# Performance work log

Measured on AMD Instinct MI355X. Metric: run time of the kernel, lower is better.

## Reference

```python
import jax, jax.numpy as jnp
import numpy as np

GROUPS = 32
HEADS = 8
EPS = 1e-5


def setup_inputs() -> dict:
    key = jax.random.key(0)
    ks = jax.random.split(key, 3)
    b, c, h, w = 8, 512, 32, 32
    x = jax.random.normal(ks[0], (b, c, h, w), dtype=jnp.float32)
    gn_w = jnp.ones((c,), jnp.float32)
    gn_b = jnp.zeros((c,), jnp.float32)
    qkv_w = jax.random.normal(ks[1], (3 * c, c), dtype=jnp.float32) * (1.0 / np.sqrt(c))
    qkv_b = jnp.zeros((3 * c,), jnp.float32)
    proj_w = jax.random.normal(ks[2], (c, c), dtype=jnp.float32) * (1.0 / np.sqrt(c))
    proj_b = jnp.zeros((c,), jnp.float32)
    return {"x": x, "gn_w": gn_w, "gn_b": gn_b, "qkv_w": qkv_w,
            "qkv_b": qkv_b, "proj_w": proj_w, "proj_b": proj_b}


def group_norm(x, weight, bias):
    b, c, h, w = x.shape
    xg = x.reshape(b, GROUPS, c // GROUPS, h, w)
    mean = xg.mean(axis=(2, 3, 4), keepdims=True)
    var = xg.var(axis=(2, 3, 4), keepdims=True)
    xn = ((xg - mean) * jax.lax.rsqrt(var + EPS)).reshape(b, c, h, w)
    return xn * weight[None, :, None, None] + bias[None, :, None, None]


def reference(x, gn_w, gn_b, qkv_w, qkv_b, proj_w, proj_b):
    b, c, h, w = x.shape
    dh = c // HEADS
    xn = group_norm(x, gn_w, gn_b)
    # 1x1 conv == per-pixel linear: (b,c,h,w) x (3c,c) -> (b,3c,h,w)
    qkv = jnp.einsum('bchw,oc->bohw', xn, qkv_w) + qkv_b[None, :, None, None]
    qkv = qkv.reshape(b, 3, HEADS, dh, h * w)  # 'three' outermost, then heads, head_dim
    q, k, v = qkv[:, 0], qkv[:, 1], qkv[:, 2]  # (b, heads, dh, hw)
    scale = dh ** (-0.5)
    attn = jax.nn.softmax(jnp.einsum('bhci,bhcj->bhij', q, k) * scale, axis=-1)
    out = jnp.einsum('bhij,bhcj->bhci', attn, v)  # (b, heads, dh, hw)
    out = out.reshape(b, c, h, w)
    out = jnp.einsum('bchw,oc->bohw', out, proj_w) + proj_b[None, :, None, None]
    return x + out
```

## Files before the change

### kernel.cpp

```cpp
#include <hip/hip_runtime.h>
#include <cstdint>
#include <cstddef>

#define BATCH 8
#define CCH   512
#define SSP   1024
#define NH    8
#define DH    64
#define O3    1536

typedef __bf16 bf16x8 __attribute__((ext_vector_type(8)));
typedef float  f32x4  __attribute__((ext_vector_type(4)));

__device__ __forceinline__ unsigned short f2bf(float f) {
    unsigned u = __builtin_bit_cast(unsigned, f);
    unsigned r = u + 0x7fffu + ((u >> 16) & 1u);
    return (unsigned short)(r >> 16);
}

__device__ __forceinline__ unsigned pk2bf(float lo, float hi) {
    unsigned ul = __builtin_bit_cast(unsigned, lo) + 0x8000u;
    unsigned uh = __builtin_bit_cast(unsigned, hi) + 0x8000u;
    return __builtin_amdgcn_perm(uh, ul, 0x07060302u);
}

__device__ __forceinline__ bf16x8 ld8(const unsigned short* p) {
    uint4 u = *(const uint4*)p;
    return __builtin_bit_cast(bf16x8, u);
}

__device__ __forceinline__ void glls16(const void* g, void* l) {
    __builtin_amdgcn_global_load_lds(
        (const __attribute__((address_space(1))) unsigned*)g,
        (__attribute__((address_space(3))) unsigned*)l, 16, 0, 0);
}

__global__ __launch_bounds__(256) void gn_wconv(const float* __restrict__ x,
                                                const float* __restrict__ gw,
                                                const float* __restrict__ gb,
                                                unsigned short* __restrict__ xnt,
                                                const float* __restrict__ s1,
                                                unsigned short* __restrict__ d1, int n1,
                                                const float* __restrict__ s2,
                                                unsigned short* __restrict__ d2) {
    int t = threadIdx.x;
    if (blockIdx.x >= 256) {
        int i = (blockIdx.x - 256) * 256 + t;
        const float4* sp;
        ushort4* dp;
        if (i < n1) { sp = (const float4*)s1 + i; dp = (ushort4*)d1 + i; }
        else        { sp = (const float4*)s2 + (i - n1); dp = (ushort4*)d2 + (i - n1); }
        float4 v = *sp;
        ushort4 o;
        o.x = f2bf(v.x); o.y = f2bf(v.y); o.z = f2bf(v.z); o.w = f2bf(v.w);
        *dp = o;
        return;
    }

    int blk = blockIdx.x;
    int b = blk >> 5, g = blk & 31;
    const float4* xp = (const float4*)(x + (size_t)(b * CCH + g * 16) * SSP);

    float4 vals[16];
    float sum = 0.f, ss = 0.f;
#pragma unroll
    for (int i = 0; i < 16; i++) {
        float4 v = xp[i * 256 + t];
        vals[i] = v;
        sum += (v.x + v.y) + (v.z + v.w);
        ss  += (v.x * v.x + v.y * v.y) + (v.z * v.z + v.w * v.w);
    }
#pragma unroll
    for (int o = 32; o; o >>= 1) {
        sum += __shfl_xor(sum, o, 64);
        ss  += __shfl_xor(ss,  o, 64);
    }
    __shared__ float red[8];
    if ((t & 63) == 0) { red[(t >> 6) * 2] = sum; red[(t >> 6) * 2 + 1] = ss; }
    __syncthreads();
    sum = red[0] + red[2] + red[4] + red[6];
    ss  = red[1] + red[3] + red[5] + red[7];

    float mean = sum * (1.f / 16384.f);
    float var  = ss * (1.f / 16384.f) - mean * mean;
    float rstd = rsqrtf(var + 1e-5f);

    __shared__ unsigned short tile[16][1032];
#pragma unroll
    for (int i = 0; i < 16; i++) {
        int f4 = i * 256 + t;
        int c = f4 >> 8;
        int s = (f4 & 255) * 4;
        float wsc = gw[g * 16 + c] * rstd;
        float bia = gb[g * 16 + c] - mean * wsc;
        float4 v = vals[i];
        tile[c][s + 0] = f2bf(v.x * wsc + bia);
        tile[c][s + 1] = f2bf(v.y * wsc + bia);
        tile[c][s + 2] = f2bf(v.z * wsc + bia);
        tile[c][s + 3] = f2bf(v.w * wsc + bia);
    }
    __syncthreads();

    int c2 = (t & 7) * 2, sr = t >> 3;
    unsigned short* outbase = xnt + (size_t)b * SSP * CCH + g * 16 + c2;
#pragma unroll
    for (int i = 0; i < 32; i++) {
        int s = i * 32 + sr;
        unsigned v = (unsigned)tile[c2][s] | ((unsigned)tile[c2 + 1][s] << 16);
        *(unsigned*)(outbase + (size_t)s * CCH) = v;
    }
}

__global__ __launch_bounds__(256) void gemm_qkv(const unsigned short* __restrict__ Aall,
                                                const unsigned short* __restrict__ Bw,
                                                const float* __restrict__ bias,
                                                unsigned short* __restrict__ Call,
                                                unsigned short* __restrict__ vtout) {
    const int K = 512;
    int bz = blockIdx.z;
    const unsigned short* A = Aall + (size_t)bz * SSP * CCH;
    int m0 = blockIdx.x * 128, n0 = blockIdx.y * 128;

    __shared__ unsigned short As[128 * 64], Bs[128 * 64];
    int t = threadIdx.x, wave = t >> 6, lane = t & 63;
    int quad = lane >> 4, l16 = lane & 15;
    int wm = (wave & 1) * 64, wn = (wave >> 1) * 64;

    int lrow = lane >> 3;
    int lc   = ((lane & 7) - lrow) & 7;
    const unsigned short* Ag = A  + (size_t)(m0 + wave * 32 + lrow) * K + lc * 8;
    const unsigned short* Bg = Bw + (size_t)(n0 + wave * 32 + lrow) * K + lc * 8;
    unsigned short* Asw = As + wave * 2048;
    unsigned short* Bsw = Bs + wave * 2048;

    f32x4 acc[4][4];
#pragma unroll
    for (int i = 0; i < 4; i++)
#pragma unroll
        for (int j = 0; j < 4; j++) acc[i][j] = f32x4{0.f, 0.f, 0.f, 0.f};

    int rowA = (wm + l16) * 64, rowB = (wn + l16) * 64;
    int cph[2];
#pragma unroll
    for (int kc = 0; kc < 2; kc++) cph[kc] = ((quad + 4 * kc + l16) & 7) * 8;

    for (int k0 = 0; k0 < K; k0 += 64) {
        __syncthreads();
#pragma unroll
        for (int i = 0; i < 4; i++) {
            glls16(Ag + (size_t)i * 8 * K + k0, Asw + i * 512);
            glls16(Bg + (size_t)i * 8 * K + k0, Bsw + i * 512);
        }
        __syncthreads();
#pragma unroll
        for (int kc = 0; kc < 2; kc++) {
            bf16x8 af[4], bfr[4];
#pragma unroll
            for (int i = 0; i < 4; i++) {
                af[i]  = ld8(As + rowA + i * 1024 + cph[kc]);
                bfr[i] = ld8(Bs + rowB + i * 1024 + cph[kc]);
            }
#pragma unroll
            for (int i = 0; i < 4; i++)
#pragma unroll
                for (int j = 0; j < 4; j++)
                    acc[i][j] = __builtin_amdgcn_mfma_f32_16x16x32_bf16(af[i], bfr[j], acc[i][j], 0, 0, 0);
        }
    }

    if (n0 < 1024) {
        float scl = (n0 < 512) ? 0.18033688011f : 1.0f;
        unsigned short* Cp = Call + (size_t)bz * SSP * O3;
#pragma unroll
        for (int i = 0; i < 4; i++)
#pragma unroll
            for (int j = 0; j < 4; j++) {
                int col = n0 + wn + j * 16 + l16;
                float bv = bias[col];
#pragma unroll
                for (int r = 0; r < 4; r++) {
                    int row = m0 + wm + i * 16 + quad * 4 + r;
                    Cp[(size_t)row * O3 + col] = f2bf((acc[i][j][r] + bv) * scl);
                }
            }
    } else {
#pragma unroll
        for (int j = 0; j < 4; j++) {
            int col = n0 + wn + j * 16 + l16;
            float bv = bias[col];
            unsigned short* vp = vtout + ((size_t)bz * 512 + (col - 1024)) * SSP;
#pragma unroll
            for (int i = 0; i < 4; i++) {
                int s = m0 + wm + i * 16 + quad * 4;
                uint2 d;
                d.x = pk2bf(acc[i][j][0] + bv, acc[i][j][1] + bv);
                d.y = pk2bf(acc[i][j][2] + bv, acc[i][j][3] + bv);
                *(uint2*)(vp + s) = d;
            }
        }
    }
}

__global__ __launch_bounds__(256) void gemm_proj(const unsigned short* __restrict__ Pw,
                                                 const unsigned short* __restrict__ Oall,
                                                 const float* __restrict__ bias,
                                                 const float* __restrict__ xres,
                                                 float* __restrict__ Out) {
    const int K = 512;
    int bz = blockIdx.z;
    const unsigned short* Bv = Oall + (size_t)bz * SSP * CCH;
    int m0 = blockIdx.x * 64, n0 = blockIdx.y * 128;

    __shared__ unsigned short As[64 * 64], Bs[128 * 64];
    int t = threadIdx.x, wave = t >> 6, lane = t & 63;
    int quad = lane >> 4, l16 = lane & 15;
    int wr = (wave & 1) * 32, wc = (wave >> 1) * 64;

    int lrow = lane >> 3;
    int lc   = ((lane & 7) - lrow) & 7;
    const unsigned short* Ag = Pw + (size_t)(m0 + wave * 16 + lrow) * K + lc * 8;
    const unsigned short* Bg = Bv + (size_t)(n0 + wave * 32 + lrow) * K + lc * 8;
    unsigned short* Asw = As + wave * 1024;
    unsigned short* Bsw = Bs + wave * 2048;

    f32x4 acc[2][4];
#pragma unroll
    for (int i = 0; i < 2; i++)
#pragma unroll
        for (int j = 0; j < 4; j++) acc[i][j] = f32x4{0.f, 0.f, 0.f, 0.f};

    int rowA = (wr + l16) * 64, rowB = (wc + l16) * 64;
    int cph[2];
#pragma unroll
    for (int kc = 0; kc < 2; kc++) cph[kc] = ((quad + 4 * kc + l16) & 7) * 8;

    for (int k0 = 0; k0 < K; k0 += 64) {
        __syncthreads();
#pragma unroll
        for (int i = 0; i < 2; i++)
            glls16(Ag + (size_t)i * 8 * K + k0, Asw + i * 512);
#pragma unroll
        for (int i = 0; i < 4; i++)
            glls16(Bg + (size_t)i * 8 * K + k0, Bsw + i * 512);
        __syncthreads();
#pragma unroll
        for (int kc = 0; kc < 2; kc++) {
            bf16x8 af[2], bfr[4];
#pragma unroll
            for (int i = 0; i < 2; i++) af[i]  = ld8(As + rowA + i * 1024 + cph[kc]);
#pragma unroll
            for (int j = 0; j < 4; j++) bfr[j] = ld8(Bs + rowB + j * 1024 + cph[kc]);
#pragma unroll
            for (int i = 0; i < 2; i++)
#pragma unroll
                for (int j = 0; j < 4; j++)
                    acc[i][j] = __builtin_amdgcn_mfma_f32_16x16x32_bf16(af[i], bfr[j], acc[i][j], 0, 0, 0);
        }
    }
#pragma unroll
    for (int i = 0; i < 2; i++)
#pragma unroll
        for (int j = 0; j < 4; j++) {
            int col = n0 + wc + j * 16 + l16;
#pragma unroll
            for (int r = 0; r < 4; r++) {
                int row = m0 + wr + i * 16 + quad * 4 + r;
                size_t idx = (size_t)bz * CCH * SSP + (size_t)row * SSP + col;
                Out[idx] = xres[idx] + acc[i][j][r] + bias[row];
            }
        }
}

__global__ __launch_bounds__(256, 2) void attn(const unsigned short* __restrict__ qkvt,
                                               const unsigned short* __restrict__ vt,
                                               unsigned short* __restrict__ ot) {
    int blk = blockIdx.x;
    int xcd = blk & 7, jj = blk >> 3;
    int bh = xcd * 8 + (jj >> 3);
    int i0 = (jj & 7) * 128;
    int b = bh >> 3, h = bh & 7;

    __shared__ unsigned short PsD[4][2][16 * 64];

    int t = threadIdx.x, wave = t >> 6, lane = t & 63;
    int quad = lane >> 4, l16 = lane & 15;

    bf16x8 qf[2][2];
#pragma unroll
    for (int is = 0; is < 2; is++) {
        const unsigned short* qp =
            qkvt + ((size_t)b * SSP + i0 + wave * 32 + is * 16 + l16) * O3 + h * DH + quad * 8;
        qf[0][is] = ld8(qp);
        qf[1][is] = ld8(qp + 32);
    }

    f32x4 Oa[2][4];
#pragma unroll
    for (int is = 0; is < 2; is++)
#pragma unroll
        for (int i = 0; i < 4; i++) Oa[is][i] = f32x4{0.f, 0.f, 0.f, 0.f};
    float l_acc[2] = {0.f, 0.f};

    const unsigned short* kbase = qkvt + (size_t)b * SSP * O3 + CCH + h * DH;
    const unsigned short* vbase = vt + (size_t)bh * DH * SSP;

    for (int jt = 0; jt < 16; jt++) {
        int j0 = jt * 64;

        bf16x8 kf[2][4];
#pragma unroll
        for (int kc = 0; kc < 2; kc++)
#pragma unroll
            for (int tj = 0; tj < 4; tj++)
                kf[kc][tj] = ld8(kbase + (size_t)(j0 + tj * 16 + l16) * O3 + kc * 32 + quad * 8);
        bf16x8 vfr[2][4];
#pragma unroll
        for (int kj = 0; kj < 2; kj++)
#pragma unroll
            for (int tc = 0; tc < 4; tc++)
                vfr[kj][tc] = ld8(vbase + (tc * 16 + l16) * SSP + j0 + kj * 32 + quad * 8);

#pragma unroll
        for (int is = 0; is < 2; is++) {
            f32x4 sc[4];
#pragma unroll
            for (int tj = 0; tj < 4; tj++) sc[tj] = f32x4{0.f, 0.f, 0.f, 0.f};
#pragma unroll
            for (int kc = 0; kc < 2; kc++)
#pragma unroll
                for (int tj = 0; tj < 4; tj++)
                    sc[tj] = __builtin_amdgcn_mfma_f32_16x16x32_bf16(kf[kc][tj], qf[kc][is], sc[tj], 0, 0, 0);

#pragma unroll
            for (int tj = 0; tj < 4; tj++)
#pragma unroll
                for (int r = 0; r < 4; r++) {
                    float p = __builtin_amdgcn_exp2f(sc[tj][r]);
                    sc[tj][r] = p;
                    l_acc[is] += p;
                }

            unsigned short* Ps = PsD[wave][is];
#pragma unroll
            for (int tj = 0; tj < 4; tj++) {
                uint2 d;
                d.x = pk2bf(sc[tj][0], sc[tj][1]);
                d.y = pk2bf(sc[tj][2], sc[tj][3]);
                int phys = (tj * 2 + (quad >> 1) + l16) & 7;
                *(uint2*)(Ps + l16 * 64 + phys * 8 + (quad & 1) * 4) = d;
            }

#pragma unroll
            for (int kj = 0; kj < 2; kj++) {
                bf16x8 pf = ld8(Ps + l16 * 64 + ((kj * 4 + quad + l16) & 7) * 8);
#pragma unroll
                for (int tc = 0; tc < 4; tc++)
                    Oa[is][tc] = __builtin_amdgcn_mfma_f32_16x16x32_bf16(vfr[kj][tc], pf, Oa[is][tc], 0, 0, 0);
            }
        }
    }

#pragma unroll
    for (int is = 0; is < 2; is++) {
        float l = l_acc[is];
        l += __shfl_xor(l, 16, 64);
        l += __shfl_xor(l, 32, 64);
        float rl = 1.f / l;
        int i = i0 + wave * 32 + is * 16 + l16;
        unsigned short* ob = ot + ((size_t)b * SSP + i) * CCH + h * DH;
#pragma unroll
        for (int tc = 0; tc < 4; tc++) {
            uint2 d;
            d.x = pk2bf(Oa[is][tc][0] * rl, Oa[is][tc][1] * rl);
            d.y = pk2bf(Oa[is][tc][2] * rl, Oa[is][tc][3] * rl);
            *(uint2*)(ob + tc * 16 + quad * 4) = d;
        }
    }
}

extern "C" void kernel_launch(void* const* d_in, const int* in_sizes, int n_in,
                              void* d_out, int out_size, void* d_ws, size_t ws_size,
                              hipStream_t stream) {
    const float* x      = (const float*)d_in[0];
    const float* gn_w   = (const float*)d_in[1];
    const float* gn_b   = (const float*)d_in[2];
    const float* qkv_w  = (const float*)d_in[3];
    const float* qkv_b  = (const float*)d_in[4];
    const float* proj_w = (const float*)d_in[5];
    const float* proj_b = (const float*)d_in[6];
    float* out = (float*)d_out;

    char* ws = (char*)d_ws;
    unsigned short* xnt   = (unsigned short*)(ws);
    unsigned short* qw_bf = (unsigned short*)(ws + 8388608);
    unsigned short* pw_bf = (unsigned short*)(ws + 9961472);
    unsigned short* qkvt  = (unsigned short*)(ws + 10485760);
    unsigned short* vt    = (unsigned short*)(ws + 35651584);
    unsigned short* otb   = (unsigned short*)(ws + 44040192);

    gn_wconv<<<dim3(1280), dim3(256), 0, stream>>>(x, gn_w, gn_b, xnt,
                                                   qkv_w, qw_bf, 196608, proj_w, pw_bf);
    gemm_qkv<<<dim3(8, 12, 8), dim3(256), 0, stream>>>(xnt, qw_bf, qkv_b, qkvt, vt);
    attn<<<dim3(512), dim3(256), 0, stream>>>(qkvt, vt, otb);
    gemm_proj<<<dim3(8, 8, 8), dim3(256), 0, stream>>>(pw_bf, otb, proj_b, x, out);
}
```

Before: 187.3 us.

## Stage K/V tiles in double-buffered LDS with async global-to-LDS loads

The attention kernel now copies each 64-key K and V tile into double-buffered shared memory with direct global-to-LDS loads (glls16), prefetching the next tile while the current one is computed. Before, every wave loaded its own K/V fragments from global memory. The two query sub-tiles are also interleaved so their MFMA chains alternate. This cuts redundant global traffic across the four waves and hides load latency, at the cost of more LDS use (32 KB extra, which may reduce occupancy) and a block barrier each iteration.

```diff
diff --git a/kernel.cpp b/kernel.cpp
--- a/kernel.cpp
+++ b/kernel.cpp
@@ -280,6 +280,8 @@
     int i0 = (jj & 7) * 128;
     int b = bh >> 3, h = bh & 7;
 
+    __shared__ unsigned short KsD[2][64 * 64];
+    __shared__ unsigned short VsD[2][64 * 64];
     __shared__ unsigned short PsD[4][2][16 * 64];
 
     int t = threadIdx.x, wave = t >> 6, lane = t & 63;
@@ -301,63 +303,95 @@
         for (int i = 0; i < 4; i++) Oa[is][i] = f32x4{0.f, 0.f, 0.f, 0.f};
     float l_acc[2] = {0.f, 0.f};
 
-    const unsigned short* kbase = qkvt + (size_t)b * SSP * O3 + CCH + h * DH;
-    const unsigned short* vbase = vt + (size_t)bh * DH * SSP;
-
-    for (int jt = 0; jt < 16; jt++) {
-        int j0 = jt * 64;
+    int lrow8 = lane >> 3, lc8 = ((lane & 7) - lrow8) & 7;
+    const unsigned short* kga = qkvt + (size_t)b * SSP * O3 + CCH + h * DH;
+    const unsigned short* vga = vt + (size_t)bh * DH * SSP;
+    size_t koff[2];
+    int voff[2], lds_off[2];
+#pragma unroll
+    for (int p = 0; p < 2; p++) {
+        int row = wave * 16 + p * 8 + lrow8;
+        koff[p] = (size_t)row * O3 + lc8 * 8;
+        voff[p] = row * SSP + lc8 * 8;
+        lds_off[p] = (wave * 16 + p * 8) * 64;
+    }
+
+#pragma unroll
+    for (int p = 0; p < 2; p++) glls16(kga + koff[p], &KsD[0][lds_off[p]]);
+#pragma unroll
+    for (int p = 0; p < 2; p++) glls16(vga + voff[p], &VsD[0][lds_off[p]]);
+    __syncthreads();
+
+    for (int jb = 0; jb < 16; jb++) {
+        int cur = jb & 1;
+        if (jb < 15) {
+            int nxt = cur ^ 1;
+            size_t j1k = (size_t)(jb + 1) * 64 * O3;
+            int j1v = (jb + 1) * 64;
+#pragma unroll
+            for (int p = 0; p < 2; p++) glls16(kga + j1k + koff[p], &KsD[nxt][lds_off[p]]);
+#pragma unroll
+            for (int p = 0; p < 2; p++) glls16(vga + j1v + voff[p], &VsD[nxt][lds_off[p]]);
+        }
+        const unsigned short* ks = KsD[cur];
+        const unsigned short* vs = VsD[cur];
 
         bf16x8 kf[2][4];
 #pragma unroll
         for (int kc = 0; kc < 2; kc++)
 #pragma unroll
-            for (int tj = 0; tj < 4; tj++)
-                kf[kc][tj] = ld8(kbase + (size_t)(j0 + tj * 16 + l16) * O3 + kc * 32 + quad * 8);
-        bf16x8 vfr[2][4];
-#pragma unroll
-        for (int kj = 0; kj < 2; kj++)
-#pragma unroll
-            for (int tc = 0; tc < 4; tc++)
-                vfr[kj][tc] = ld8(vbase + (tc * 16 + l16) * SSP + j0 + kj * 32 + quad * 8);
-
-#pragma unroll
-        for (int is = 0; is < 2; is++) {
-            f32x4 sc[4];
-#pragma unroll
-            for (int tj = 0; tj < 4; tj++) sc[tj] = f32x4{0.f, 0.f, 0.f, 0.f};
-#pragma unroll
-            for (int kc = 0; kc < 2; kc++)
-#pragma unroll
-                for (int tj = 0; tj < 4; tj++)
-                    sc[tj] = __builtin_amdgcn_mfma_f32_16x16x32_bf16(kf[kc][tj], qf[kc][is], sc[tj], 0, 0, 0);
-
-#pragma unroll
-            for (int tj = 0; tj < 4; tj++)
-#pragma unroll
-                for (int r = 0; r < 4; r++) {
-                    float p = __builtin_amdgcn_exp2f(sc[tj][r]);
-                    sc[tj][r] = p;
-                    l_acc[is] += p;
-                }
-
-            unsigned short* Ps = PsD[wave][is];
-#pragma unroll
             for (int tj = 0; tj < 4; tj++) {
-                uint2 d;
-                d.x = pk2bf(sc[tj][0], sc[tj][1]);
-                d.y = pk2bf(sc[tj][2], sc[tj][3]);
-                int phys = (tj * 2 + (quad >> 1) + l16) & 7;
-                *(uint2*)(Ps + l16 * 64 + phys * 8 + (quad & 1) * 4) = d;
-            }
-
-#pragma unroll
-            for (int kj = 0; kj < 2; kj++) {
-                bf16x8 pf = ld8(Ps + l16 * 64 + ((kj * 4 + quad + l16) & 7) * 8);
-#pragma unroll
-                for (int tc = 0; tc < 4; tc++)
-                    Oa[is][tc] = __builtin_amdgcn_mfma_f32_16x16x32_bf16(vfr[kj][tc], pf, Oa[is][tc], 0, 0, 0);
-            }
-        }
+                int row = tj * 16 + l16;
+                kf[kc][tj] = ld8(ks + row * 64 + ((kc * 4 + quad + l16) & 7) * 8);
+            }
+
+        f32x4 sc0[4], sc1[4];
+#pragma unroll
+        for (int tj = 0; tj < 4; tj++) { sc0[tj] = f32x4{0.f,0.f,0.f,0.f}; sc1[tj] = f32x4{0.f,0.f,0.f,0.f}; }
+#pragma unroll
+        for (int kc = 0; kc < 2; kc++)
+#pragma unroll
+            for (int tj = 0; tj < 4; tj++) {
+                sc0[tj] = __builtin_amdgcn_mfma_f32_16x16x32_bf16(kf[kc][tj], qf[kc][0], sc0[tj], 0, 0, 0);
+                sc1[tj] = __builtin_amdgcn_mfma_f32_16x16x32_bf16(kf[kc][tj], qf[kc][1], sc1[tj], 0, 0, 0);
+            }
+
+        unsigned short* Ps0 = PsD[wave][0];
+        unsigned short* Ps1 = PsD[wave][1];
+#pragma unroll
+        for (int tj = 0; tj < 4; tj++) {
+#pragma unroll
+            for (int r = 0; r < 4; r++) {
+                float p0 = __builtin_amdgcn_exp2f(sc0[tj][r]);
+                float p1 = __builtin_amdgcn_exp2f(sc1[tj][r]);
+                sc0[tj][r] = p0; l_acc[0] += p0;
+                sc1[tj][r] = p1; l_acc[1] += p1;
+            }
+            int phys = (tj * 2 + (quad >> 1) + l16) & 7;
+            uint2 d0, d1;
+            d0.x = pk2bf(sc0[tj][0], sc0[tj][1]);
+            d0.y = pk2bf(sc0[tj][2], sc0[tj][3]);
+            d1.x = pk2bf(sc1[tj][0], sc1[tj][1]);
+            d1.y = pk2bf(sc1[tj][2], sc1[tj][3]);
+            *(uint2*)(Ps0 + l16 * 64 + phys * 8 + (quad & 1) * 4) = d0;
+            *(uint2*)(Ps1 + l16 * 64 + phys * 8 + (quad & 1) * 4) = d1;
+        }
+
+#pragma unroll
+        for (int kj = 0; kj < 2; kj++) {
+            int pch = ((kj * 4 + quad + l16) & 7) * 8;
+            bf16x8 pf0 = ld8(Ps0 + l16 * 64 + pch);
+            bf16x8 pf1 = ld8(Ps1 + l16 * 64 + pch);
+#pragma unroll
+            for (int tc = 0; tc < 4; tc++) {
+                int row = tc * 16 + l16;
+                bf16x8 vf = ld8(vs + row * 64 + ((kj * 4 + quad + l16) & 7) * 8);
+                Oa[0][tc] = __builtin_amdgcn_mfma_f32_16x16x32_bf16(vf, pf0, Oa[0][tc], 0, 0, 0);
+                Oa[1][tc] = __builtin_amdgcn_mfma_f32_16x16x32_bf16(vf, pf1, Oa[1][tc], 0, 0, 0);
+            }
+        }
+
+        __syncthreads();
     }
 
 #pragma unroll
```

New measurement: 153.6 us. 18.0% less time.
